# Performance work log

Measured on AMD Instinct MI355X. Metric: run time of the kernel, lower is better.

The kernel has to match this reference:

```python
import jax, jax.numpy as jnp
import numpy as np


def setup_inputs() -> dict:
    key = jax.random.key(0)
    k1, k2, k3, k4 = jax.random.split(key, 4)
    B, S, H = 4, 2048, 1024
    Ha, P = 1024, 1024
    x = jax.random.normal(k1, (B, S, H), dtype=jnp.float32)
    score_weights = jax.random.normal(k2, (B, S, S), dtype=jnp.float32)
    W_c = jax.random.normal(k3, (H, 3 * Ha), dtype=jnp.float32) * 0.02
    b_c = jnp.zeros((3 * Ha,), dtype=jnp.float32)
    W_p = jax.random.normal(k4, (Ha, P), dtype=jnp.float32) * 0.02
    b_p = jnp.zeros((P,), dtype=jnp.float32)
    return {"x": x, "score_weights": score_weights, "W_c": W_c, "b_c": b_c, "W_p": W_p, "b_p": b_p}


def reference(x, score_weights, W_c, b_c, W_p, b_p):
    # fused QKV projection: [B,S,H] @ [H,3*Ha] + b -> [B,S,3*Ha]
    c = jnp.einsum("bsh,hf->bsf", x, W_c) + b_c
    Ha = c.shape[-1] // 3
    query, key, value = jnp.split(c, 3, axis=2)  # each [B,S,Ha]
    # scaled dot-product scores [B,S,S] with additive bias
    scale = jax.lax.rsqrt(jnp.asarray(Ha, dtype=x.dtype))
    scores = jnp.einsum("bqd,bkd->bqk", query, key) * scale + score_weights
    probs = jax.nn.softmax(scores, axis=-1)
    context = jnp.einsum("bqk,bkd->bqd", probs, value)  # [B,S,Ha]
    # output projection [B,S,Ha] @ [Ha,P] + b -> [B,S,P]
    return jnp.einsum("bsd,dp->bsp", context, W_p) + b_p
```

## Files before the change

### kernel.cpp

```cpp
#include <hip/hip_runtime.h>
#include <hip/hip_bf16.h>
#include <cstdint>

typedef __attribute__((ext_vector_type(8))) short v8s;
typedef __attribute__((ext_vector_type(4))) float v4f;

__device__ __forceinline__ unsigned short f32_to_bf16(float f) {
  unsigned int u = __builtin_bit_cast(unsigned int, f);
  u += 0x7fffu + ((u >> 16) & 1u);
  return (unsigned short)(u >> 16);
}

__device__ __forceinline__ void gload_lds16(const void* g, void* l) {
  __builtin_amdgcn_global_load_lds((const __attribute__((address_space(1))) void*)g,
                                   (__attribute__((address_space(3))) void*)l, 16, 0, 0);
}

enum { EPI_BF16_BIAS = 0, EPI_F32_BIAS = 1, EPI_F32_SCALE_ADD = 2 };

template <int MODE>
__global__ __launch_bounds__(256)
void gemm_nt(const unsigned short* __restrict__ A, long long strideA, int lda,
             const unsigned short* __restrict__ B, long long strideB, int ldb,
             void* __restrict__ Cout, long long strideC, int ldc,
             const float* __restrict__ bias,
             const float* __restrict__ addmat, long long strideAdd,
             float scale, int K)
{
  __shared__ __attribute__((aligned(16))) short smA[128 * 64];
  __shared__ __attribute__((aligned(16))) short smB[128 * 64];

  const int tid  = threadIdx.x;
  const int lane = tid & 63;
  const int wave = tid >> 6;
  const int wm = wave >> 1, wn = wave & 1;
  const int bz = blockIdx.z;
  const int tileM = blockIdx.y * 128, tileN = blockIdx.x * 128;

  const unsigned short* Ag = A + (long long)bz * strideA + (long long)tileM * lda;
  const unsigned short* Bg = B + (long long)bz * strideB + (long long)tileN * ldb;

  const int l8    = lane >> 3;
  const int srcCb = (lane & 7) ^ l8;

  v4f acc[4][4] = {};

  for (int k0 = 0; k0 < K; k0 += 64) {
    #pragma unroll
    for (int i = 0; i < 4; ++i) {
      const int c   = wave * 4 + i;
      const int row = c * 8 + l8;
      gload_lds16(Ag + (long long)row * lda + k0 + srcCb * 8, &smA[c * 512]);
      gload_lds16(Bg + (long long)row * ldb + k0 + srcCb * 8, &smB[c * 512]);
    }
    __syncthreads();
    #pragma unroll
    for (int kk = 0; kk < 2; ++kk) {
      v8s af[4], bf[4];
      #pragma unroll
      for (int f = 0; f < 4; ++f) {
        const int rA = wm * 64 + f * 16 + (lane & 15);
        const int cA = (kk * 4 + (lane >> 4)) ^ (rA & 7);
        af[f] = *(const v8s*)&smA[rA * 64 + cA * 8];
        const int rB = wn * 64 + f * 16 + (lane & 15);
        const int cB = (kk * 4 + (lane >> 4)) ^ (rB & 7);
        bf[f] = *(const v8s*)&smB[rB * 64 + cB * 8];
      }
      #pragma unroll
      for (int fm = 0; fm < 4; ++fm)
        #pragma unroll
        for (int fn = 0; fn < 4; ++fn)
          acc[fm][fn] = __builtin_amdgcn_mfma_f32_16x16x32_bf16(af[fm], bf[fn], acc[fm][fn], 0, 0, 0);
    }
    __syncthreads();
  }

  const int row0 = tileM + wm * 64 + (lane >> 4) * 4;
  const int col0 = tileN + wn * 64 + (lane & 15);
  #pragma unroll
  for (int fm = 0; fm < 4; ++fm) {
    #pragma unroll
    for (int fn = 0; fn < 4; ++fn) {
      const int col = col0 + fn * 16;
      #pragma unroll
      for (int r = 0; r < 4; ++r) {
        const int row = row0 + fm * 16 + r;
        const float v = acc[fm][fn][r];
        if (MODE == EPI_F32_SCALE_ADD) {
          float* C = (float*)Cout + (long long)bz * strideC;
          const float* Wt = addmat + (long long)bz * strideAdd;
          C[(long long)row * ldc + col] = v * scale + Wt[(long long)row * ldc + col];
        } else if (MODE == EPI_F32_BIAS) {
          float* C = (float*)Cout + (long long)bz * strideC;
          C[(long long)row * ldc + col] = v + bias[col];
        } else {
          unsigned short* C = (unsigned short*)Cout + (long long)bz * strideC;
          const float b = bias ? bias[col] : 0.0f;
          C[(long long)row * ldc + col] = f32_to_bf16(v + b);
        }
      }
    }
  }
}

__global__ __launch_bounds__(256)
void cvt_f32_bf16_kernel(const float* __restrict__ in, unsigned short* __restrict__ out,
                         long long n)
{
  const long long i = ((long long)blockIdx.x * 256 + threadIdx.x) * 4;
  if (i >= n) return;
  const float4 v = *(const float4*)(in + i);
  typedef __attribute__((ext_vector_type(4))) unsigned short v4us;
  v4us o;
  o.x = f32_to_bf16(v.x); o.y = f32_to_bf16(v.y);
  o.z = f32_to_bf16(v.z); o.w = f32_to_bf16(v.w);
  *(v4us*)(out + i) = o;
}

__global__ __launch_bounds__(256)
void transpose_f32_bf16_kernel(const float* __restrict__ in, unsigned short* __restrict__ out,
                               int R, int C)
{
  __shared__ float t[32][33];
  const int c0 = blockIdx.x * 32, r0 = blockIdx.y * 32;
  const int tx = threadIdx.x, ty = threadIdx.y;
  for (int i = ty; i < 32; i += 8)
    t[i][tx] = in[(long long)(r0 + i) * C + (c0 + tx)];
  __syncthreads();
  for (int i = ty; i < 32; i += 8)
    out[(long long)(c0 + i) * R + (r0 + tx)] = f32_to_bf16(t[tx][i]);
}

__global__ __launch_bounds__(256)
void transpose_bf16_kernel(const unsigned short* __restrict__ in, long long strideIn, int ldin,
                           unsigned short* __restrict__ out, long long strideOut,
                           int R)
{
  __shared__ unsigned short t[32][33];
  const unsigned short* src = in + (long long)blockIdx.z * strideIn;
  unsigned short* dst = out + (long long)blockIdx.z * strideOut;
  const int c0 = blockIdx.x * 32, r0 = blockIdx.y * 32;
  const int tx = threadIdx.x, ty = threadIdx.y;
  for (int i = ty; i < 32; i += 8)
    t[i][tx] = src[(long long)(r0 + i) * ldin + (c0 + tx)];
  __syncthreads();
  for (int i = ty; i < 32; i += 8)
    dst[(long long)(c0 + i) * R + (r0 + tx)] = t[tx][i];
}

__global__ __launch_bounds__(256)
void softmax_rows(const float* __restrict__ scores, unsigned short* __restrict__ probs)
{
  const long long row = blockIdx.x;
  const float* src = scores + row * 2048;
  unsigned short* dst = probs + row * 2048;
  const int t = threadIdx.x;
  float v[8];
  const float4 a = *(const float4*)(src + t * 8);
  const float4 b = *(const float4*)(src + t * 8 + 4);
  v[0]=a.x; v[1]=a.y; v[2]=a.z; v[3]=a.w; v[4]=b.x; v[5]=b.y; v[6]=b.z; v[7]=b.w;

  float m = v[0];
  #pragma unroll
  for (int j = 1; j < 8; ++j) m = fmaxf(m, v[j]);
  for (int o = 32; o; o >>= 1) m = fmaxf(m, __shfl_xor(m, o));
  __shared__ float redm[4], reds[4];
  if ((t & 63) == 0) redm[t >> 6] = m;
  __syncthreads();
  m = fmaxf(fmaxf(redm[0], redm[1]), fmaxf(redm[2], redm[3]));

  float s = 0.f;
  #pragma unroll
  for (int j = 0; j < 8; ++j) { v[j] = __expf(v[j] - m); s += v[j]; }
  for (int o = 32; o; o >>= 1) s += __shfl_xor(s, o);
  if ((t & 63) == 0) reds[t >> 6] = s;
  __syncthreads();
  s = reds[0] + reds[1] + reds[2] + reds[3];
  const float inv = 1.0f / s;

  v8s o8;
  #pragma unroll
  for (int j = 0; j < 8; ++j) o8[j] = (short)f32_to_bf16(v[j] * inv);
  *(v8s*)(dst + t * 8) = o8;
}

extern "C" void kernel_launch(void* const* d_in, const int* in_sizes, int n_in,
                              void* d_out, int out_size, void* d_ws, size_t ws_size,
                              hipStream_t stream) {
  (void)in_sizes; (void)n_in; (void)out_size; (void)ws_size;
  const float* x   = (const float*)d_in[0];
  const float* sw  = (const float*)d_in[1];
  const float* W_c = (const float*)d_in[2];
  const float* b_c = (const float*)d_in[3];
  const float* W_p = (const float*)d_in[4];
  const float* b_p = (const float*)d_in[5];
  float* out = (float*)d_out;

  const int Bb = 4, S = 2048, H = 1024, Ha = 1024, P = 1024;
  const int M = Bb * S;
  char* ws = (char*)d_ws;
  const long long MB = 1024LL * 1024LL;
  float*          scores = (float*)(ws + 0);
  unsigned short* x_bf   = (unsigned short*)(ws + 0);
  unsigned short* ctx    = (unsigned short*)(ws + 0);
  unsigned short* probs  = (unsigned short*)(ws + 64 * MB);
  unsigned short* qkv    = (unsigned short*)(ws + 96 * MB);
  unsigned short* Vt     = (unsigned short*)(ws + 144 * MB);
  unsigned short* Wc_t   = (unsigned short*)(ws + 160 * MB);
  unsigned short* Wp_t   = (unsigned short*)(ws + 166 * MB);

  const dim3 tb(32, 8);

  cvt_f32_bf16_kernel<<<(unsigned)((long long)M * H / 4 / 256), 256, 0, stream>>>(
      x, x_bf, (long long)M * H);
  transpose_f32_bf16_kernel<<<dim3(3 * Ha / 32, H / 32), tb, 0, stream>>>(W_c, Wc_t, H, 3 * Ha);
  transpose_f32_bf16_kernel<<<dim3(P / 32, Ha / 32), tb, 0, stream>>>(W_p, Wp_t, Ha, P);
  gemm_nt<EPI_BF16_BIAS><<<dim3(3 * Ha / 128, M / 128, 1), 256, 0, stream>>>(
      x_bf, 0, H, Wc_t, 0, H, qkv, 0, 3 * Ha, b_c, nullptr, 0, 0.f, H);
  gemm_nt<EPI_F32_SCALE_ADD><<<dim3(S / 128, S / 128, Bb), 256, 0, stream>>>(
      qkv, (long long)S * 3 * Ha, 3 * Ha,
      qkv + Ha, (long long)S * 3 * Ha, 3 * Ha,
      scores, (long long)S * S, S, nullptr, sw, (long long)S * S, 0.03125f, Ha);
  softmax_rows<<<Bb * S, 256, 0, stream>>>(scores, probs);
  transpose_bf16_kernel<<<dim3(Ha / 32, S / 32, Bb), tb, 0, stream>>>(
      qkv + 2 * Ha, (long long)S * 3 * Ha, 3 * Ha, Vt, (long long)Ha * S, S);
  gemm_nt<EPI_BF16_BIAS><<<dim3(Ha / 128, S / 128, Bb), 256, 0, stream>>>(
      probs, (long long)S * S, S, Vt, (long long)Ha * S, S,
      ctx, (long long)S * Ha, Ha, nullptr, nullptr, 0, 0.f, S);
  gemm_nt<EPI_F32_BIAS><<<dim3(P / 128, M / 128, 1), 256, 0, stream>>>(
      ctx, 0, Ha, Wp_t, 0, Ha, out, 0, P, b_p, nullptr, 0, 0.f, Ha);
}
```

Before: 270.7 us.

## Replace 128x128 GEMM with double-buffered 256x256 eight-wave pipelined kernel

Swaps the single-buffered 128x128 tile GEMM for a 256x256 tile kernel with 512 threads. It double-buffers LDS and interleaves global-to-LDS prefetches of the next K tiles across eight MFMA phases, using explicit barriers, vmcnt waits and s_setprio. The aim is to raise data reuse per tile and hide global load latency behind matrix math. In exchange, LDS use and register pressure per block rise sharply, and the smaller GEMMs launch only 128 blocks, which may underfill the GPU.

```diff
diff --git a/kernel.cpp b/kernel.cpp
--- a/kernel.cpp
+++ b/kernel.cpp
@@ -18,67 +18,111 @@
 
 enum { EPI_BF16_BIAS = 0, EPI_F32_BIAS = 1, EPI_F32_SCALE_ADD = 2 };
 
+#define SG_A(bufi, half, rowoff, tau) \
+  gload_lds16(Ag + (long long)((half)*128 + (rowoff) + rS) * lda + (long long)(tau)*64 + swz, \
+              &smA[bufi][half][(rowoff) + wb][0])
+#define SG_B(bufi, half, rowoff, tau) \
+  gload_lds16(Bg + (long long)((half)*128 + (rowoff) + rS) * ldb + (long long)(tau)*64 + swz, \
+              &smB[bufi][half][(rowoff) + wb][0])
+
+#define PHASE(bufi, fmh, kk, READB, STAGES, TAILS) \
+  { \
+    v8s afr[4]; \
+    _Pragma("unroll") \
+    for (int j = 0; j < 4; ++j) { \
+      const int r = ((fmh)*4 + j)*16 + l15; \
+      afr[j] = *(const v8s*)&smA[bufi][wm][r][(((kk)*4 + l4) ^ (r & 7)) * 8]; \
+    } \
+    if (READB) { \
+      _Pragma("unroll") \
+      for (int j = 0; j < 4; ++j) { \
+        const int r = wn64 + j*16 + l15; \
+        bfr[kk][j] = *(const v8s*)&smB[bufi][wnh][r][(((kk)*4 + l4) ^ (r & 7)) * 8]; \
+      } \
+    } \
+    STAGES \
+    __builtin_amdgcn_s_barrier(); \
+    asm volatile("s_waitcnt lgkmcnt(0)" ::: "memory"); \
+    __builtin_amdgcn_s_setprio(1); \
+    _Pragma("unroll") \
+    for (int j = 0; j < 4; ++j) { \
+      _Pragma("unroll") \
+      for (int fn = 0; fn < 4; ++fn) \
+        acc[(fmh)*4 + j][fn] = __builtin_amdgcn_mfma_f32_16x16x32_bf16( \
+            afr[j], bfr[kk][fn], acc[(fmh)*4 + j][fn], 0, 0, 0); \
+    } \
+    __builtin_amdgcn_s_setprio(0); \
+    TAILS \
+    __builtin_amdgcn_s_barrier(); \
+  }
+
 template <int MODE>
-__global__ __launch_bounds__(256)
-void gemm_nt(const unsigned short* __restrict__ A, long long strideA, int lda,
+__global__ __launch_bounds__(512, 2)
+void gemm256(const unsigned short* __restrict__ A, long long strideA, int lda,
              const unsigned short* __restrict__ B, long long strideB, int ldb,
              void* __restrict__ Cout, long long strideC, int ldc,
              const float* __restrict__ bias,
              const float* __restrict__ addmat, long long strideAdd,
              float scale, int K)
 {
-  __shared__ __attribute__((aligned(16))) short smA[128 * 64];
-  __shared__ __attribute__((aligned(16))) short smB[128 * 64];
+  __shared__ __attribute__((aligned(16))) short smA[2][2][128][64];
+  __shared__ __attribute__((aligned(16))) short smB[2][2][128][64];
 
   const int tid  = threadIdx.x;
   const int lane = tid & 63;
   const int wave = tid >> 6;
-  const int wm = wave >> 1, wn = wave & 1;
-  const int bz = blockIdx.z;
-  const int tileM = blockIdx.y * 128, tileN = blockIdx.x * 128;
-
-  const unsigned short* Ag = A + (long long)bz * strideA + (long long)tileM * lda;
-  const unsigned short* Bg = B + (long long)bz * strideB + (long long)tileN * ldb;
-
-  const int l8    = lane >> 3;
-  const int srcCb = (lane & 7) ^ l8;
-
-  v4f acc[4][4] = {};
-
-  for (int k0 = 0; k0 < K; k0 += 64) {
-    #pragma unroll
-    for (int i = 0; i < 4; ++i) {
-      const int c   = wave * 4 + i;
-      const int row = c * 8 + l8;
-      gload_lds16(Ag + (long long)row * lda + k0 + srcCb * 8, &smA[c * 512]);
-      gload_lds16(Bg + (long long)row * ldb + k0 + srcCb * 8, &smB[c * 512]);
-    }
-    __syncthreads();
-    #pragma unroll
-    for (int kk = 0; kk < 2; ++kk) {
-      v8s af[4], bf[4];
-      #pragma unroll
-      for (int f = 0; f < 4; ++f) {
-        const int rA = wm * 64 + f * 16 + (lane & 15);
-        const int cA = (kk * 4 + (lane >> 4)) ^ (rA & 7);
-        af[f] = *(const v8s*)&smA[rA * 64 + cA * 8];
-        const int rB = wn * 64 + f * 16 + (lane & 15);
-        const int cB = (kk * 4 + (lane >> 4)) ^ (rB & 7);
-        bf[f] = *(const v8s*)&smB[rB * 64 + cB * 8];
-      }
-      #pragma unroll
-      for (int fm = 0; fm < 4; ++fm)
-        #pragma unroll
-        for (int fn = 0; fn < 4; ++fn)
-          acc[fm][fn] = __builtin_amdgcn_mfma_f32_16x16x32_bf16(af[fm], bf[fn], acc[fm][fn], 0, 0, 0);
-    }
-    __syncthreads();
+  const int wm   = wave >> 2;
+  const int wn   = wave & 3;
+  const int wnh  = wn >> 1;
+  const int wn64 = (wn & 1) * 64;
+  const int l15  = lane & 15, l4 = lane >> 4;
+  const int bz   = blockIdx.z;
+  const long long tileM = (long long)blockIdx.y * 256;
+  const long long tileN = (long long)blockIdx.x * 256;
+
+  const unsigned short* Ag = A + (long long)bz * strideA + tileM * lda;
+  const unsigned short* Bg = B + (long long)bz * strideB + tileN * ldb;
+
+  const int rS  = tid >> 3;
+  const int swz = ((tid & 7) ^ ((tid >> 3) & 7)) * 8;
+  const int wb  = wave * 8;
+
+  v4f acc[8][4] = {};
+  v8s bfr[2][4];
+
+  const int nt    = K >> 6;
+  const int niter = nt >> 1;
+
+  SG_A(0, 0, 0, 0);  SG_A(0, 1, 0, 0);
+  SG_A(0, 0, 64, 0); SG_A(0, 1, 64, 0);
+  SG_B(0, 0, 0, 0);  SG_B(0, 0, 64, 0);
+  SG_B(0, 1, 0, 0);  SG_B(0, 1, 64, 0);
+  SG_A(1, 0, 0, 1);  SG_A(1, 1, 0, 1);
+  SG_B(1, 0, 0, 1);  SG_B(1, 0, 64, 1);
+  asm volatile("s_waitcnt vmcnt(4)" ::: "memory");
+  __builtin_amdgcn_s_barrier();
+
+  for (int i = 0; i < niter; ++i) {
+    const int t1 = 2 * i + 1, t2 = 2 * i + 2, t3 = 2 * i + 3;
+    const bool more = (i + 1 < niter);
+
+    PHASE(0, 0, 0, 1, { SG_B(1, 1, 0, t1); SG_B(1, 1, 64, t1); }, {})
+    PHASE(0, 0, 1, 1, { SG_A(1, 0, 64, t1); SG_A(1, 1, 64, t1); }, {})
+    PHASE(0, 1, 0, 0, { if (more) { SG_A(0, 0, 0, t2); SG_A(0, 1, 0, t2); } }, {})
+    PHASE(0, 1, 1, 0, { if (more) { SG_B(0, 0, 0, t2); SG_B(0, 0, 64, t2); } },
+          { if (more) { asm volatile("s_waitcnt vmcnt(4)" ::: "memory"); }
+            else      { asm volatile("s_waitcnt vmcnt(0)" ::: "memory"); } })
+    PHASE(1, 0, 0, 1, { if (more) { SG_B(0, 1, 0, t2); SG_B(0, 1, 64, t2); } }, {})
+    PHASE(1, 0, 1, 1, { if (more) { SG_A(0, 0, 64, t2); SG_A(0, 1, 64, t2); } }, {})
+    PHASE(1, 1, 0, 0, { if (more) { SG_A(1, 0, 0, t3); SG_A(1, 1, 0, t3); } }, {})
+    PHASE(1, 1, 1, 0, { if (more) { SG_B(1, 0, 0, t3); SG_B(1, 0, 64, t3); } },
+          { if (more) { asm volatile("s_waitcnt vmcnt(4)" ::: "memory"); } })
   }
 
-  const int row0 = tileM + wm * 64 + (lane >> 4) * 4;
-  const int col0 = tileN + wn * 64 + (lane & 15);
-  #pragma unroll
-  for (int fm = 0; fm < 4; ++fm) {
+  const int row0 = (int)tileM + wm * 128 + l4 * 4;
+  const int col0 = (int)tileN + wn * 64 + l15;
+  #pragma unroll
+  for (int fm = 0; fm < 8; ++fm) {
     #pragma unroll
     for (int fn = 0; fn < 4; ++fn) {
       const int col = col0 + fn * 16;
@@ -215,18 +259,18 @@
       x, x_bf, (long long)M * H);
   transpose_f32_bf16_kernel<<<dim3(3 * Ha / 32, H / 32), tb, 0, stream>>>(W_c, Wc_t, H, 3 * Ha);
   transpose_f32_bf16_kernel<<<dim3(P / 32, Ha / 32), tb, 0, stream>>>(W_p, Wp_t, Ha, P);
-  gemm_nt<EPI_BF16_BIAS><<<dim3(3 * Ha / 128, M / 128, 1), 256, 0, stream>>>(
+  gemm256<EPI_BF16_BIAS><<<dim3(3 * Ha / 256, M / 256, 1), 512, 0, stream>>>(
       x_bf, 0, H, Wc_t, 0, H, qkv, 0, 3 * Ha, b_c, nullptr, 0, 0.f, H);
-  gemm_nt<EPI_F32_SCALE_ADD><<<dim3(S / 128, S / 128, Bb), 256, 0, stream>>>(
+  gemm256<EPI_F32_SCALE_ADD><<<dim3(S / 256, S / 256, Bb), 512, 0, stream>>>(
       qkv, (long long)S * 3 * Ha, 3 * Ha,
       qkv + Ha, (long long)S * 3 * Ha, 3 * Ha,
       scores, (long long)S * S, S, nullptr, sw, (long long)S * S, 0.03125f, Ha);
   softmax_rows<<<Bb * S, 256, 0, stream>>>(scores, probs);
   transpose_bf16_kernel<<<dim3(Ha / 32, S / 32, Bb), tb, 0, stream>>>(
       qkv + 2 * Ha, (long long)S * 3 * Ha, 3 * Ha, Vt, (long long)Ha * S, S);
-  gemm_nt<EPI_BF16_BIAS><<<dim3(Ha / 128, S / 128, Bb), 256, 0, stream>>>(
+  gemm256<EPI_BF16_BIAS><<<dim3(Ha / 256, S / 256, Bb), 512, 0, stream>>>(
       probs, (long long)S * S, S, Vt, (long long)Ha * S, S,
       ctx, (long long)S * Ha, Ha, nullptr, nullptr, 0, 0.f, S);
-  gemm_nt<EPI_F32_BIAS><<<dim3(P / 128, M / 128, 1), 256, 0, stream>>>(
+  gemm256<EPI_F32_BIAS><<<dim3(P / 256, M / 256, 1), 512, 0, stream>>>(
       ctx, 0, Ha, Wp_t, 0, Ha, out, 0, P, b_p, nullptr, 0, 0.f, Ha);
 }
```

Measured after the change: 322.9 us. 1.19x slower.

## Add 256x256 eight-wave GEMM with phased LDS pipeline for QKV and scores

Applied to the files above, without the earlier changes.

Introduces a new GEMM kernel with 256x256 tiles, 512 threads, and double-buffered LDS filled by direct global-to-LDS loads. The main loop is split into phases that interleave the next tile's loads with MFMA work, using explicit vmcnt waits, barriers and setprio. The QKV projection and score GEMMs switch to this kernel to get more data reuse per tile and better load/compute overlap. In exchange, register and LDS use per block go up. The larger tiles also give fewer blocks, which could hurt occupancy or leave the grid unevenly balanced across CUs.

```diff
diff --git a/kernel.cpp b/kernel.cpp
--- a/kernel.cpp
+++ b/kernel.cpp
@@ -103,6 +103,149 @@
   }
 }
 
+
+#define WAITVM(n) asm volatile("s_waitcnt vmcnt(" #n ")" ::: "memory")
+
+#define STG_A(bufi, fmh, t) do { \
+  gload_lds16(Ag + (long long)(gA0 + (fmh) * 64) * lda + (long long)(t) * 64 + swz, \
+              &smA[bufi][hW][(fmh) * 64 + dA0][0]); \
+  gload_lds16(Ag + (long long)(gA0 + 8 + (fmh) * 64) * lda + (long long)(t) * 64 + swz, \
+              &smA[bufi][hW][(fmh) * 64 + dA0 + 8][0]); \
+} while (0)
+
+#define STG_B(bufi, fnh, t) do { \
+  gload_lds16(Bg + (long long)(gB0 + (fnh) * 32) * ldb + (long long)(t) * 64 + swz, \
+              &smB[bufi][hW][dB0 + (fnh) * 32][0]); \
+  gload_lds16(Bg + (long long)(gB0 + 8 + (fnh) * 32) * ldb + (long long)(t) * 64 + swz, \
+              &smB[bufi][hW][dB0 + (fnh) * 32 + 8][0]); \
+} while (0)
+
+#define PH(bufi, fmh, fnh, DOA, STAGE, TAIL) \
+  { \
+    if (DOA) { \
+      _Pragma("unroll") \
+      for (int j = 0; j < 4; ++j) { \
+        afr[j][0] = *(const v8s*)&smA[bufi][wm][(fmh) * 64 + j * 16 + l15][((0 + l4) ^ l7) * 8]; \
+        afr[j][1] = *(const v8s*)&smA[bufi][wm][(fmh) * 64 + j * 16 + l15][((4 + l4) ^ l7) * 8]; \
+      } \
+    } \
+    v8s b00 = *(const v8s*)&smB[bufi][wnh][wn64 + ((fnh) * 2 + 0) * 16 + l15][((0 + l4) ^ l7) * 8]; \
+    v8s b01 = *(const v8s*)&smB[bufi][wnh][wn64 + ((fnh) * 2 + 0) * 16 + l15][((4 + l4) ^ l7) * 8]; \
+    v8s b10 = *(const v8s*)&smB[bufi][wnh][wn64 + ((fnh) * 2 + 1) * 16 + l15][((0 + l4) ^ l7) * 8]; \
+    v8s b11 = *(const v8s*)&smB[bufi][wnh][wn64 + ((fnh) * 2 + 1) * 16 + l15][((4 + l4) ^ l7) * 8]; \
+    STAGE; \
+    __builtin_amdgcn_s_barrier(); \
+    asm volatile("s_waitcnt lgkmcnt(0)" ::: "memory"); \
+    __builtin_amdgcn_s_setprio(1); \
+    _Pragma("unroll") \
+    for (int j = 0; j < 4; ++j) { \
+      acc[(fmh) * 4 + j][(fnh) * 2 + 0] = __builtin_amdgcn_mfma_f32_16x16x32_bf16(afr[j][0], b00, acc[(fmh) * 4 + j][(fnh) * 2 + 0], 0, 0, 0); \
+      acc[(fmh) * 4 + j][(fnh) * 2 + 0] = __builtin_amdgcn_mfma_f32_16x16x32_bf16(afr[j][1], b01, acc[(fmh) * 4 + j][(fnh) * 2 + 0], 0, 0, 0); \
+      acc[(fmh) * 4 + j][(fnh) * 2 + 1] = __builtin_amdgcn_mfma_f32_16x16x32_bf16(afr[j][0], b10, acc[(fmh) * 4 + j][(fnh) * 2 + 1], 0, 0, 0); \
+      acc[(fmh) * 4 + j][(fnh) * 2 + 1] = __builtin_amdgcn_mfma_f32_16x16x32_bf16(afr[j][1], b11, acc[(fmh) * 4 + j][(fnh) * 2 + 1], 0, 0, 0); \
+    } \
+    __builtin_amdgcn_s_setprio(0); \
+    TAIL; \
+    __builtin_amdgcn_s_barrier(); \
+  }
+
+template <int MODE>
+__global__ __launch_bounds__(512, 2)
+void gemm256v2(const unsigned short* __restrict__ A, long long strideA, int lda,
+               const unsigned short* __restrict__ B, long long strideB, int ldb,
+               void* __restrict__ Cout, long long strideC, int ldc,
+               const float* __restrict__ bias,
+               const float* __restrict__ addmat, long long strideAdd,
+               float scale, int K)
+{
+  __shared__ __attribute__((aligned(16))) short smA[2][2][128][64];
+  __shared__ __attribute__((aligned(16))) short smB[2][2][128][64];
+
+  const int tid  = threadIdx.x;
+  const int lane = tid & 63;
+  const int wave = tid >> 6;
+  const int wm   = wave >> 2;
+  const int wn   = wave & 3;
+  const int wnh  = wn >> 1;
+  const int wn64 = (wn & 1) * 64;
+  const int l15  = lane & 15, l4 = lane >> 4, l7 = lane & 7;
+  const int bz   = blockIdx.z;
+  const long long tileM = (long long)blockIdx.y * 256;
+  const long long tileN = (long long)blockIdx.x * 256;
+
+  const unsigned short* Ag = A + (long long)bz * strideA + tileM * lda;
+  const unsigned short* Bg = B + (long long)bz * strideB + tileN * ldb;
+
+  const int hW  = wave >> 2;
+  const int dA0 = (wave & 3) * 16;
+  const int gA0 = hW * 128 + dA0 + (lane >> 3);
+  const int dB0 = ((wave >> 1) & 1) * 64 + (wave & 1) * 16;
+  const int gB0 = hW * 128 + dB0 + (lane >> 3);
+  const int swz = ((lane & 7) ^ ((lane >> 3) & 7)) * 8;
+
+  v4f acc[8][4] = {};
+  v8s afr[4][2];
+
+  const int nt    = K >> 6;
+  const int niter = nt >> 1;
+
+  STG_A(0, 0, 0); STG_B(0, 0, 0);
+  STG_A(0, 1, 0); STG_B(0, 1, 0);
+  STG_A(1, 0, 1); STG_B(1, 0, 1);
+  WAITVM(8);
+  __builtin_amdgcn_s_barrier();
+
+  for (int i = 0; i < niter - 1; ++i) {
+    const int o = 2 * i + 1, e2 = 2 * i + 2, o2 = 2 * i + 3;
+    PH(0, 0, 0, 1, STG_A(1, 1, o),  WAITVM(6))
+    PH(0, 0, 1, 0, STG_B(1, 1, o),  (void)0)
+    PH(0, 1, 0, 1, STG_A(0, 0, e2), (void)0)
+    PH(0, 1, 1, 0, STG_B(0, 0, e2), WAITVM(8))
+    PH(1, 0, 0, 1, STG_A(0, 1, e2), WAITVM(6))
+    PH(1, 0, 1, 0, STG_B(0, 1, e2), (void)0)
+    PH(1, 1, 0, 1, STG_A(1, 0, o2), (void)0)
+    PH(1, 1, 1, 0, STG_B(1, 0, o2), WAITVM(8))
+  }
+  {
+    const int o = nt - 1;
+    PH(0, 0, 0, 1, STG_A(1, 1, o), WAITVM(6))
+    PH(0, 0, 1, 0, STG_B(1, 1, o), (void)0)
+    PH(0, 1, 0, 1, (void)0,        (void)0)
+    PH(0, 1, 1, 0, (void)0,        WAITVM(4))
+    PH(1, 0, 0, 1, (void)0,        WAITVM(0))
+    PH(1, 0, 1, 0, (void)0,        (void)0)
+    PH(1, 1, 0, 1, (void)0,        (void)0)
+    PH(1, 1, 1, 0, (void)0,        (void)0)
+  }
+
+  const int row0 = (int)tileM + wm * 128 + (lane >> 4) * 4;
+  const int col0 = (int)tileN + wn * 64 + l15;
+  #pragma unroll
+  for (int fm = 0; fm < 8; ++fm) {
+    #pragma unroll
+    for (int fn = 0; fn < 4; ++fn) {
+      const int col = col0 + fn * 16;
+      #pragma unroll
+      for (int r = 0; r < 4; ++r) {
+        const int row = row0 + fm * 16 + r;
+        const float v = acc[fm][fn][r];
+        if (MODE == EPI_F32_SCALE_ADD) {
+          float* C = (float*)Cout + (long long)bz * strideC;
+          const float* Wt = addmat + (long long)bz * strideAdd;
+          C[(long long)row * ldc + col] = v * scale + Wt[(long long)row * ldc + col];
+        } else if (MODE == EPI_F32_BIAS) {
+          float* C = (float*)Cout + (long long)bz * strideC;
+          C[(long long)row * ldc + col] = v + bias[col];
+        } else {
+          unsigned short* C = (unsigned short*)Cout + (long long)bz * strideC;
+          const float b = bias ? bias[col] : 0.0f;
+          C[(long long)row * ldc + col] = f32_to_bf16(v + b);
+        }
+      }
+    }
+  }
+}
+
 __global__ __launch_bounds__(256)
 void cvt_f32_bf16_kernel(const float* __restrict__ in, unsigned short* __restrict__ out,
                          long long n)
@@ -215,9 +358,9 @@
       x, x_bf, (long long)M * H);
   transpose_f32_bf16_kernel<<<dim3(3 * Ha / 32, H / 32), tb, 0, stream>>>(W_c, Wc_t, H, 3 * Ha);
   transpose_f32_bf16_kernel<<<dim3(P / 32, Ha / 32), tb, 0, stream>>>(W_p, Wp_t, Ha, P);
-  gemm_nt<EPI_BF16_BIAS><<<dim3(3 * Ha / 128, M / 128, 1), 256, 0, stream>>>(
+  gemm256v2<EPI_BF16_BIAS><<<dim3(3 * Ha / 256, M / 256, 1), 512, 0, stream>>>(
       x_bf, 0, H, Wc_t, 0, H, qkv, 0, 3 * Ha, b_c, nullptr, 0, 0.f, H);
-  gemm_nt<EPI_F32_SCALE_ADD><<<dim3(S / 128, S / 128, Bb), 256, 0, stream>>>(
+  gemm256v2<EPI_F32_SCALE_ADD><<<dim3(S / 256, S / 256, Bb), 512, 0, stream>>>(
       qkv, (long long)S * 3 * Ha, 3 * Ha,
       qkv + Ha, (long long)S * 3 * Ha, 3 * Ha,
       scores, (long long)S * S, S, nullptr, sw, (long long)S * S, 0.03125f, Ha);
```

After: 297.7 us. +10.0%, slower.

## Double-buffer GEMM LDS tiles and fuse V transpose into QKV epilogue

Applied to the files above, without the earlier changes.

Adds a two-stage LDS buffer to the bf16 MFMA GEMM so the next K tile is fetched while the current one is computed, with one barrier per iteration. Makes the QKV projection write the V columns directly in transposed layout, removing the separate bf16 transpose kernel and its extra memory pass. This doubles the shared memory used per block, which may lower occupancy. It also relies on the barrier to ensure asynchronous LDS loads have completed.

```diff
diff --git a/kernel.cpp b/kernel.cpp
--- a/kernel.cpp
+++ b/kernel.cpp
@@ -25,10 +25,11 @@
              void* __restrict__ Cout, long long strideC, int ldc,
              const float* __restrict__ bias,
              const float* __restrict__ addmat, long long strideAdd,
-             float scale, int K)
-{
-  __shared__ __attribute__((aligned(16))) short smA[128 * 64];
-  __shared__ __attribute__((aligned(16))) short smB[128 * 64];
+             float scale, int K,
+             unsigned short* __restrict__ VtOut)
+{
+  __shared__ __attribute__((aligned(16))) short smA[2][128 * 64];
+  __shared__ __attribute__((aligned(16))) short smB[2][128 * 64];
 
   const int tid  = threadIdx.x;
   const int lane = tid & 63;
@@ -44,16 +45,26 @@
   const int srcCb = (lane & 7) ^ l8;
 
   v4f acc[4][4] = {};
-
-  for (int k0 = 0; k0 < K; k0 += 64) {
-    #pragma unroll
-    for (int i = 0; i < 4; ++i) {
-      const int c   = wave * 4 + i;
-      const int row = c * 8 + l8;
-      gload_lds16(Ag + (long long)row * lda + k0 + srcCb * 8, &smA[c * 512]);
-      gload_lds16(Bg + (long long)row * ldb + k0 + srcCb * 8, &smB[c * 512]);
-    }
-    __syncthreads();
+  const int nt = K >> 6;
+
+#define STAGE128(buf, t) do { \
+    _Pragma("unroll") \
+    for (int i_ = 0; i_ < 4; ++i_) { \
+      const int c_   = wave * 4 + i_; \
+      const int row_ = c_ * 8 + l8; \
+      gload_lds16(Ag + (long long)row_ * lda + (long long)(t) * 64 + srcCb * 8, \
+                  &smA[buf][c_ * 512]); \
+      gload_lds16(Bg + (long long)row_ * ldb + (long long)(t) * 64 + srcCb * 8, \
+                  &smB[buf][c_ * 512]); \
+    } \
+  } while (0)
+
+  STAGE128(0, 0);
+  __syncthreads();
+
+  for (int t = 0; t < nt; ++t) {
+    const int cur = t & 1;
+    if (t + 1 < nt) STAGE128(cur ^ 1, t + 1);
     #pragma unroll
     for (int kk = 0; kk < 2; ++kk) {
       v8s af[4], bf[4];
@@ -61,10 +72,10 @@
       for (int f = 0; f < 4; ++f) {
         const int rA = wm * 64 + f * 16 + (lane & 15);
         const int cA = (kk * 4 + (lane >> 4)) ^ (rA & 7);
-        af[f] = *(const v8s*)&smA[rA * 64 + cA * 8];
+        af[f] = *(const v8s*)&smA[cur][rA * 64 + cA * 8];
         const int rB = wn * 64 + f * 16 + (lane & 15);
         const int cB = (kk * 4 + (lane >> 4)) ^ (rB & 7);
-        bf[f] = *(const v8s*)&smB[rB * 64 + cB * 8];
+        bf[f] = *(const v8s*)&smB[cur][rB * 64 + cB * 8];
       }
       #pragma unroll
       for (int fm = 0; fm < 4; ++fm)
@@ -74,29 +85,46 @@
     }
     __syncthreads();
   }
+#undef STAGE128
 
   const int row0 = tileM + wm * 64 + (lane >> 4) * 4;
   const int col0 = tileN + wn * 64 + (lane & 15);
+  const bool vtActive = (MODE == EPI_BF16_BIAS) && (VtOut != nullptr) && (tileN >= 2048);
+
   #pragma unroll
   for (int fm = 0; fm < 4; ++fm) {
     #pragma unroll
     for (int fn = 0; fn < 4; ++fn) {
       const int col = col0 + fn * 16;
-      #pragma unroll
-      for (int r = 0; r < 4; ++r) {
-        const int row = row0 + fm * 16 + r;
-        const float v = acc[fm][fn][r];
-        if (MODE == EPI_F32_SCALE_ADD) {
-          float* C = (float*)Cout + (long long)bz * strideC;
-          const float* Wt = addmat + (long long)bz * strideAdd;
-          C[(long long)row * ldc + col] = v * scale + Wt[(long long)row * ldc + col];
-        } else if (MODE == EPI_F32_BIAS) {
-          float* C = (float*)Cout + (long long)bz * strideC;
-          C[(long long)row * ldc + col] = v + bias[col];
-        } else {
-          unsigned short* C = (unsigned short*)Cout + (long long)bz * strideC;
-          const float b = bias ? bias[col] : 0.0f;
-          C[(long long)row * ldc + col] = f32_to_bf16(v + b);
+      if (vtActive) {
+        const int rowb = row0 + fm * 16;
+        const int d = col - 2048;
+        const int b = rowb >> 11;
+        const int s0 = rowb & 2047;
+        const float bb = bias[col];
+        ushort4 w;
+        w.x = f32_to_bf16(acc[fm][fn][0] + bb);
+        w.y = f32_to_bf16(acc[fm][fn][1] + bb);
+        w.z = f32_to_bf16(acc[fm][fn][2] + bb);
+        w.w = f32_to_bf16(acc[fm][fn][3] + bb);
+        *(ushort4*)&VtOut[((long long)b * 1024 + d) * 2048 + s0] = w;
+      } else {
+        #pragma unroll
+        for (int r = 0; r < 4; ++r) {
+          const int row = row0 + fm * 16 + r;
+          const float v = acc[fm][fn][r];
+          if (MODE == EPI_F32_SCALE_ADD) {
+            float* C = (float*)Cout + (long long)bz * strideC;
+            const float* Wt = addmat + (long long)bz * strideAdd;
+            C[(long long)row * ldc + col] = v * scale + Wt[(long long)row * ldc + col];
+          } else if (MODE == EPI_F32_BIAS) {
+            float* C = (float*)Cout + (long long)bz * strideC;
+            C[(long long)row * ldc + col] = v + bias[col];
+          } else {
+            unsigned short* C = (unsigned short*)Cout + (long long)bz * strideC;
+            const float b = bias ? bias[col] : 0.0f;
+            C[(long long)row * ldc + col] = f32_to_bf16(v + b);
+          }
         }
       }
     }
@@ -129,23 +157,6 @@
   __syncthreads();
   for (int i = ty; i < 32; i += 8)
     out[(long long)(c0 + i) * R + (r0 + tx)] = f32_to_bf16(t[tx][i]);
-}
-
-__global__ __launch_bounds__(256)
-void transpose_bf16_kernel(const unsigned short* __restrict__ in, long long strideIn, int ldin,
-                           unsigned short* __restrict__ out, long long strideOut,
-                           int R)
-{
-  __shared__ unsigned short t[32][33];
-  const unsigned short* src = in + (long long)blockIdx.z * strideIn;
-  unsigned short* dst = out + (long long)blockIdx.z * strideOut;
-  const int c0 = blockIdx.x * 32, r0 = blockIdx.y * 32;
-  const int tx = threadIdx.x, ty = threadIdx.y;
-  for (int i = ty; i < 32; i += 8)
-    t[i][tx] = src[(long long)(r0 + i) * ldin + (c0 + tx)];
-  __syncthreads();
-  for (int i = ty; i < 32; i += 8)
-    dst[(long long)(c0 + i) * R + (r0 + tx)] = t[tx][i];
 }
 
 __global__ __launch_bounds__(256)
@@ -216,17 +227,15 @@
   transpose_f32_bf16_kernel<<<dim3(3 * Ha / 32, H / 32), tb, 0, stream>>>(W_c, Wc_t, H, 3 * Ha);
   transpose_f32_bf16_kernel<<<dim3(P / 32, Ha / 32), tb, 0, stream>>>(W_p, Wp_t, Ha, P);
   gemm_nt<EPI_BF16_BIAS><<<dim3(3 * Ha / 128, M / 128, 1), 256, 0, stream>>>(
-      x_bf, 0, H, Wc_t, 0, H, qkv, 0, 3 * Ha, b_c, nullptr, 0, 0.f, H);
+      x_bf, 0, H, Wc_t, 0, H, qkv, 0, 3 * Ha, b_c, nullptr, 0, 0.f, H, Vt);
   gemm_nt<EPI_F32_SCALE_ADD><<<dim3(S / 128, S / 128, Bb), 256, 0, stream>>>(
       qkv, (long long)S * 3 * Ha, 3 * Ha,
       qkv + Ha, (long long)S * 3 * Ha, 3 * Ha,
-      scores, (long long)S * S, S, nullptr, sw, (long long)S * S, 0.03125f, Ha);
+      scores, (long long)S * S, S, nullptr, sw, (long long)S * S, 0.03125f, Ha, nullptr);
   softmax_rows<<<Bb * S, 256, 0, stream>>>(scores, probs);
-  transpose_bf16_kernel<<<dim3(Ha / 32, S / 32, Bb), tb, 0, stream>>>(
-      qkv + 2 * Ha, (long long)S * 3 * Ha, 3 * Ha, Vt, (long long)Ha * S, S);
   gemm_nt<EPI_BF16_BIAS><<<dim3(Ha / 128, S / 128, Bb), 256, 0, stream>>>(
       probs, (long long)S * S, S, Vt, (long long)Ha * S, S,
-      ctx, (long long)S * Ha, Ha, nullptr, nullptr, 0, 0.f, S);
+      ctx, (long long)S * Ha, Ha, nullptr, nullptr, 0, 0.f, S, nullptr);
   gemm_nt<EPI_F32_BIAS><<<dim3(P / 128, M / 128, 1), 256, 0, stream>>>(
-      ctx, 0, Ha, Wp_t, 0, Ha, out, 0, P, b_p, nullptr, 0, 0.f, Ha);
-}
+      ctx, 0, Ha, Wp_t, 0, Ha, out, 0, P, b_p, nullptr, 0, 0.f, Ha, nullptr);
+}
```

Measured after the change: 253.3 us. 6.5% less time.
